# Optimization experiments

Measured on AMD Instinct MI355X. Metric: run time of the kernel, lower is better.

Reference implementation:

```python
import jax, jax.numpy as jnp
import numpy as np

HIDDEN = 1152
NUM_HEADS = 16
HEAD_DIM = HIDDEN // NUM_HEADS  # 72
BATCH, SEQ = 8, 1024


def setup_inputs() -> dict:
    key = jax.random.key(0)
    ks = jax.random.split(key, 9)
    s = 0.02
    return {
        "x": jax.random.normal(ks[0], (BATCH, SEQ, HIDDEN), dtype=jnp.float32),
        "wq": jax.random.normal(ks[1], (HIDDEN, HIDDEN), dtype=jnp.float32) * s,
        "bq": jax.random.normal(ks[2], (HIDDEN,), dtype=jnp.float32) * s,
        "wk": jax.random.normal(ks[3], (HIDDEN, HIDDEN), dtype=jnp.float32) * s,
        "bk": jax.random.normal(ks[4], (HIDDEN,), dtype=jnp.float32) * s,
        "wv": jax.random.normal(ks[5], (HIDDEN, HIDDEN), dtype=jnp.float32) * s,
        "bv": jax.random.normal(ks[6], (HIDDEN,), dtype=jnp.float32) * s,
        "wo": jax.random.normal(ks[7], (HIDDEN, HIDDEN), dtype=jnp.float32) * s,
        "bo": jax.random.normal(ks[8], (HIDDEN,), dtype=jnp.float32) * s,
    }


def reference(x, wq, bq, wk, bk, wv, bv, wo, bo):
    B, S, H = x.shape
    nh, hd = NUM_HEADS, HEAD_DIM
    # projections (weights stored [in, out] to match nn.Linear x @ W^T with W^T precomposed)
    q = (x @ wq + bq).reshape(B, S, nh, hd).transpose(0, 2, 1, 3)  # [B,nh,S,hd]
    k = (x @ wk + bk).reshape(B, S, nh, hd).transpose(0, 2, 1, 3)
    v = (x @ wv + bv).reshape(B, S, nh, hd).transpose(0, 2, 1, 3)
    scale = 1.0 / jnp.sqrt(jnp.asarray(hd, dtype=x.dtype))
    scores = jnp.einsum("bhqd,bhkd->bhqk", q, k) * scale  # [B,nh,S,S]
    attn = jax.nn.softmax(scores, axis=-1)
    out = jnp.einsum("bhqk,bhkd->bhqd", attn, v)  # [B,nh,S,hd]
    out = out.transpose(0, 2, 1, 3).reshape(B, S, H)
    return out @ wo + bo
```

## Files before the change

### kernel.cpp

```cpp
#include <hip/hip_runtime.h>
#include <hip/hip_bf16.h>

#define HIDDEN 1152
#define NUM_HEADS 16
#define BATCH 8
#define SEQ 1024
#define MROWS (BATCH * SEQ)
#define KSTRIDE 104
#define QSCALE_L2E (0.11785113019775793f * 1.4426950408889634f)

typedef __attribute__((ext_vector_type(8))) short short8;
typedef __attribute__((ext_vector_type(4))) float f32x4;

__device__ inline short f2bf(float x) {
  unsigned u = __float_as_uint(x);
  unsigned r = (u + 0x7FFFu + ((u >> 16) & 1u)) >> 16;
  return (short)(r & 0xFFFFu);
}

__device__ inline float fexp2(float x) { return __builtin_exp2f(x); }

__device__ inline void gload16(const void* g, void* l) {
  __builtin_amdgcn_global_load_lds(
      (const __attribute__((address_space(1))) void*)g,
      (__attribute__((address_space(3))) void*)l, 16, 0, 0);
}

__global__ __launch_bounds__(256) void k_prep(const float* __restrict__ X,
                                              short* __restrict__ Xb,
                                              short* __restrict__ Kp,
                                              short* __restrict__ Vt) {
  const int bid = blockIdx.x;
  if (bid < 4608) {
    const size_t base = ((size_t)bid * 256 + threadIdx.x) * 8;
    float4 a = *(const float4*)(X + base);
    float4 b = *(const float4*)(X + base + 4);
    short8 o = {f2bf(a.x), f2bf(a.y), f2bf(a.z), f2bf(a.w),
                f2bf(b.x), f2bf(b.y), f2bf(b.z), f2bf(b.w)};
    *(short8*)(Xb + base) = o;
  } else if (bid < 5120) {
    const int r = (bid - 4608) * 256 + threadIdx.x;
    const short8 z = {0, 0, 0, 0, 0, 0, 0, 0};
    short* p = Kp + (size_t)r * KSTRIDE + 72;
    *(short8*)(p) = z;
    *(short8*)(p + 8) = z;
    *(short8*)(p + 16) = z;
  } else {
    const int t = (bid - 5120) * 256 + threadIdx.x;
    const int bh = t >> 10;
    const int off = (t & 1023) * 8;
    const short o = ((t & 1023) >> 7) == 0 ? (short)0x3F80 : (short)0;
    short8 v = {o, o, o, o, o, o, o, o};
    *(short8*)(Vt + (size_t)bh * 81920 + 73728 + off) = v;
  }
}

__global__ __launch_bounds__(256) void k_cvtw(const float* __restrict__ W0,
                                              const float* __restrict__ W1,
                                              const float* __restrict__ W2,
                                              const float* __restrict__ W3,
                                              short* __restrict__ Wt) {
  __shared__ float T[64][65];
  const float* W = (blockIdx.z == 0) ? W0 : (blockIdx.z == 1) ? W1
                 : (blockIdx.z == 2) ? W2 : W3;
  short* dst = Wt + (size_t)blockIdx.z * HIDDEN * HIDDEN;
  const int n0 = blockIdx.x * 64, k0 = blockIdx.y * 64;
  const int tid = threadIdx.x;
  for (int t = tid; t < 4096; t += 256) {
    int r = t >> 6, c = t & 63;
    T[r][c] = W[(size_t)(k0 + r) * HIDDEN + n0 + c];
  }
  __syncthreads();
  for (int t = tid; t < 4096; t += 256) {
    int r = t >> 6, c = t & 63;
    dst[(size_t)(n0 + r) * HIDDEN + k0 + c] = f2bf(T[c][r]);
  }
}

__global__ __launch_bounds__(512) void k_gemm_qkv(
    const short* __restrict__ A, const short* __restrict__ Bt,
    const float* __restrict__ bq, const float* __restrict__ bk,
    const float* __restrict__ bv, short* __restrict__ Qb,
    short* __restrict__ Kp, short* __restrict__ Vt) {
  __shared__ __align__(16) short SM[24576];
  short* As = SM;
  short* Bs = SM + 16384;
  const int tid = threadIdx.x;
  const int lane = tid & 63;
  const int wid = tid >> 6;
  const int wr = wid >> 1, wc = wid & 1;
  const int flat = blockIdx.y * 27 + blockIdx.x;
  const int rid = (flat & 7) * 108 + (flat >> 3);
  const int row0 = (rid / 27) << 8;
  const int colTile = rid % 27;
  const int col0 = colTile << 7;
  const int l15 = lane & 15, lh = lane >> 4;
  const int lr8 = lane >> 3;
  const int csrc = ((lane & 7) ^ lr8) << 3;

  const f32x4 fz = {0.f, 0.f, 0.f, 0.f};
  f32x4 acc[4][4];
#pragma unroll
  for (int m = 0; m < 4; ++m)
#pragma unroll
    for (int n = 0; n < 4; ++n) acc[m][n] = fz;

  for (int k0 = 0; k0 < HIDDEN; k0 += 64) {
#pragma unroll
    for (int i = 0; i < 4; ++i) {
      const int c = (wid << 2) + i;
      const int r = (c << 3) + lr8;
      gload16(A + (size_t)(row0 + r) * HIDDEN + k0 + csrc, (void*)(As + (c << 9)));
    }
#pragma unroll
    for (int i = 0; i < 2; ++i) {
      const int c = (wid << 1) + i;
      const int r = (c << 3) + lr8;
      gload16(Bt + (size_t)(col0 + r) * HIDDEN + k0 + csrc, (void*)(Bs + (c << 9)));
    }
    __syncthreads();
#pragma unroll
    for (int ks = 0; ks < 2; ++ks) {
      short8 af[4], bfr[4];
#pragma unroll
      for (int m = 0; m < 4; ++m) {
        const int r = (wr << 6) + (m << 4) + l15;
        const int off = ((ks << 6) + (lh << 4)) ^ ((r & 7) << 4);
        af[m] = *(const short8*)((const char*)As + r * 128 + off);
      }
#pragma unroll
      for (int n = 0; n < 4; ++n) {
        const int r = (wc << 6) + (n << 4) + l15;
        const int off = ((ks << 6) + (lh << 4)) ^ ((r & 7) << 4);
        bfr[n] = *(const short8*)((const char*)Bs + r * 128 + off);
      }
      __builtin_amdgcn_s_setprio(1);
#pragma unroll
      for (int m = 0; m < 4; ++m)
#pragma unroll
        for (int n = 0; n < 4; ++n)
          acc[m][n] = __builtin_amdgcn_mfma_f32_16x16x32_bf16(af[m], bfr[n], acc[m][n], 0, 0, 0);
      __builtin_amdgcn_s_setprio(0);
    }
    __syncthreads();
  }

  const int cseg = colTile / 9;
  const int cwithin = (colTile % 9) << 7;
  if (cseg < 2) {
    short* dst = (cseg == 0) ? Qb : Kp;
    const float* bias = (cseg == 0) ? bq : bk;
    const float scl = (cseg == 0) ? QSCALE_L2E : 1.0f;
    const int rstride = (cseg == 0) ? 72 : KSTRIDE;
#pragma unroll
    for (int n = 0; n < 4; ++n) {
      const int c = cwithin + (wc << 6) + (n << 4) + l15;
      const int h = c / 72;
      const int d = c - h * 72;
      const float bvx = bias[c];
#pragma unroll
      for (int m = 0; m < 4; ++m)
#pragma unroll
        for (int i = 0; i < 4; ++i) {
          const int r = row0 + (wr << 6) + (m << 4) + (lh << 2) + i;
          const int b = r >> 10, s = r & 1023;
          dst[(size_t)((((b << 4) + h) << 10) + s) * rstride + d] =
              f2bf((acc[m][n][i] + bvx) * scl);
        }
    }
  } else {
    const int b = row0 >> 10;
    const int sb = row0 & 1023;
    short* Td = SM;
#pragma unroll
    for (int p = 0; p < 2; ++p) {
      if (wc == p) {
#pragma unroll
        for (int n = 0; n < 4; ++n) {
          const int ci = n * 16 + l15;
          const float bvx = bv[cwithin + p * 64 + ci];
#pragma unroll
          for (int m = 0; m < 4; ++m) {
            const int r0 = (wr << 6) + (m << 4) + (lh << 2);
            short4 o;
            o.x = f2bf(acc[m][n][0] + bvx);
            o.y = f2bf(acc[m][n][1] + bvx);
            o.z = f2bf(acc[m][n][2] + bvx);
            o.w = f2bf(acc[m][n][3] + bvx);
            *(short4*)(Td + ci * 264 + r0) = o;
          }
        }
      }
      __syncthreads();
      {
        const int ci = tid >> 3;
        const int part = tid & 7;
        const int cg = cwithin + p * 64 + ci;
        const int h = cg / 72;
        const int d = cg - h * 72;
        short* dstp = Vt + (((size_t)(((b << 4) + h) * 80 + d)) << 10) + sb + part * 32;
        const short* srcp = Td + ci * 264 + part * 32;
#pragma unroll
        for (int k = 0; k < 4; ++k)
          *(short8*)(dstp + k * 8) = *(const short8*)(srcp + k * 8);
      }
      __syncthreads();
    }
  }
}

__global__ __launch_bounds__(256) void k_gemm_o(const short* __restrict__ A,
                                                const short* __restrict__ Bt,
                                                const float* __restrict__ bias,
                                                float* __restrict__ C) {
  __shared__ __align__(16) short As[8192];
  __shared__ __align__(16) short Bs[8192];
  const int tid = threadIdx.x;
  const int lane = tid & 63;
  const int wid = tid >> 6;
  const int wr = wid >> 1, wc = wid & 1;
  const int flat = blockIdx.y * 9 + blockIdx.x;
  const int rid = (flat & 7) * 72 + (flat >> 3);
  const int row0 = (rid / 9) << 7;
  const int col0 = (rid % 9) << 7;
  const int l15 = lane & 15, lh = lane >> 4;
  const int lr8 = lane >> 3;
  const int csrc = ((lane & 7) ^ lr8) << 3;

  const f32x4 fz = {0.f, 0.f, 0.f, 0.f};
  f32x4 acc[4][4];
#pragma unroll
  for (int m = 0; m < 4; ++m)
#pragma unroll
    for (int n = 0; n < 4; ++n) acc[m][n] = fz;

  for (int k0 = 0; k0 < HIDDEN; k0 += 64) {
#pragma unroll
    for (int i = 0; i < 4; ++i) {
      const int chunk = (wid << 2) + i;
      const int r = (chunk << 3) + lr8;
      gload16(A + (size_t)(row0 + r) * HIDDEN + k0 + csrc, (void*)(As + (chunk << 9)));
      gload16(Bt + (size_t)(col0 + r) * HIDDEN + k0 + csrc, (void*)(Bs + (chunk << 9)));
    }
    __syncthreads();
#pragma unroll
    for (int ks = 0; ks < 2; ++ks) {
      short8 af[4], bfr[4];
#pragma unroll
      for (int m = 0; m < 4; ++m) {
        const int r = (wr << 6) + (m << 4) + l15;
        const int off = ((ks << 6) + (lh << 4)) ^ ((r & 7) << 4);
        af[m] = *(const short8*)((const char*)As + r * 128 + off);
      }
#pragma unroll
      for (int n = 0; n < 4; ++n) {
        const int r = (wc << 6) + (n << 4) + l15;
        const int off = ((ks << 6) + (lh << 4)) ^ ((r & 7) << 4);
        bfr[n] = *(const short8*)((const char*)Bs + r * 128 + off);
      }
      __builtin_amdgcn_s_setprio(1);
#pragma unroll
      for (int m = 0; m < 4; ++m)
#pragma unroll
        for (int n = 0; n < 4; ++n)
          acc[m][n] = __builtin_amdgcn_mfma_f32_16x16x32_bf16(af[m], bfr[n], acc[m][n], 0, 0, 0);
      __builtin_amdgcn_s_setprio(0);
    }
    __syncthreads();
  }

#pragma unroll
  for (int n = 0; n < 4; ++n) {
    const int c = col0 + (wc << 6) + (n << 4) + l15;
    const float bvx = bias[c];
#pragma unroll
    for (int m = 0; m < 4; ++m)
#pragma unroll
      for (int i = 0; i < 4; ++i) {
        const int r = row0 + (wr << 6) + (m << 4) + (lh << 2) + i;
        C[(size_t)r * HIDDEN + c] = acc[m][n][i] + bvx;
      }
  }
}

__global__ __launch_bounds__(256, 4) void k_attn(const short* __restrict__ Qg,
                                                 const short* __restrict__ Kp,
                                                 const short* __restrict__ Vt,
                                                 short* __restrict__ Og) {
  __shared__ __align__(16) short Ks[64 * KSTRIDE];
  __shared__ __align__(16) short Vs[80 * 64];
  __shared__ __align__(16) short Ps[4 * 16 * 72];
  const int tid = threadIdx.x, lane = tid & 63, wid = tid >> 6;
  const int l15 = lane & 15, lh = lane >> 4;
  const int id = blockIdx.x;
  const int rid = (id & 7) * 128 + (id >> 3);
  const int bh = rid >> 3;
  const int q0 = (rid & 7) << 7;
  const short8 sz = {0, 0, 0, 0, 0, 0, 0, 0};
  const f32x4 fz = {0.f, 0.f, 0.f, 0.f};

  short8 qf[2][3];
#pragma unroll
  for (int m = 0; m < 2; ++m)
#pragma unroll
    for (int ks = 0; ks < 3; ++ks) {
      const int row = q0 + wid * 32 + m * 16 + l15;
      const int e0 = ks * 32 + lh * 8;
      if (e0 < 72)
        qf[m][ks] = *(const short8*)(Qg + ((size_t)bh * 1024 + row) * 72 + e0);
      else
        qf[m][ks] = sz;
    }

  float mrun[2] = {-1e30f, -1e30f};
  f32x4 oacc[2][5];
#pragma unroll
  for (int m = 0; m < 2; ++m)
#pragma unroll
    for (int no = 0; no < 5; ++no) oacc[m][no] = fz;

  const char* kgb = (const char*)Kp + ((size_t)bh * 1024) * (KSTRIDE * 2);
  const char* vgb = (const char*)Vt + (size_t)bh * 163840;

  for (int kt = 0; kt < 16; ++kt) {
    const char* kg = kgb + (size_t)kt * 64 * (KSTRIDE * 2);
    for (int c = wid; c < 13; c += 4)
      gload16(kg + c * 1024 + lane * 16, (char*)Ks + c * 1024);
    for (int c = wid; c < 10; c += 4) {
      const int p = c * 1024 + lane * 16;
      const int d = p >> 7;
      const int sc16 = (lane & 7) ^ (d & 7);
      gload16(vgb + (size_t)d * 2048 + kt * 128 + sc16 * 16, (char*)Vs + c * 1024);
    }
    __syncthreads();

#pragma unroll
    for (int m = 0; m < 2; ++m) {
      f32x4 sa[4];
#pragma unroll
      for (int n = 0; n < 4; ++n) sa[n] = fz;
#pragma unroll
      for (int ks = 0; ks < 3; ++ks) {
        short8 kf[4];
#pragma unroll
        for (int n = 0; n < 4; ++n)
          kf[n] = *(const short8*)((const char*)Ks + (n * 16 + l15) * 208 + ks * 64 + lh * 16);
        __builtin_amdgcn_s_setprio(1);
#pragma unroll
        for (int n = 0; n < 4; ++n)
          sa[n] = __builtin_amdgcn_mfma_f32_16x16x32_bf16(kf[n], qf[m][ks], sa[n], 0, 0, 0);
        __builtin_amdgcn_s_setprio(0);
      }

#define M3(a, b, c) fmaxf(fmaxf((a), (b)), (c))
      float t0 = M3(sa[0][0], sa[0][1], sa[0][2]);
      float t1 = M3(sa[0][3], sa[1][0], sa[1][1]);
      float t2 = M3(sa[1][2], sa[1][3], sa[2][0]);
      float t3 = M3(sa[2][1], sa[2][2], sa[2][3]);
      float t4 = M3(sa[3][0], sa[3][1], sa[3][2]);
      float mx = fmaxf(M3(t0, t1, sa[3][3]), M3(t2, t3, t4));
#undef M3

      if (__any(mx > mrun[m] + 8.0f)) {
        mx = fmaxf(mx, __shfl_xor(mx, 16));
        mx = fmaxf(mx, __shfl_xor(mx, 32));
        const float nm = fmaxf(mrun[m], mx);
        const float corr = fexp2(mrun[m] - nm);
        mrun[m] = nm;
        float c0 = __shfl(corr, lh * 4 + 0);
        float c1 = __shfl(corr, lh * 4 + 1);
        float c2 = __shfl(corr, lh * 4 + 2);
        float c3 = __shfl(corr, lh * 4 + 3);
        const f32x4 cv = {c0, c1, c2, c3};
#pragma unroll
        for (int no = 0; no < 5; ++no) oacc[m][no] *= cv;
      }

#pragma unroll
      for (int n = 0; n < 4; ++n)
#pragma unroll
        for (int i = 0; i < 4; ++i) sa[n][i] = fexp2(sa[n][i] - mrun[m]);

#pragma unroll
      for (int n = 0; n < 4; ++n) {
        unsigned w0 = __builtin_amdgcn_perm(__float_as_uint(sa[n][1]),
                                            __float_as_uint(sa[n][0]), 0x07060302u);
        unsigned w1 = __builtin_amdgcn_perm(__float_as_uint(sa[n][3]),
                                            __float_as_uint(sa[n][2]), 0x07060302u);
        uint2 w = {w0, w1};
        *(uint2*)((char*)Ps + wid * 2304 + l15 * 144 + n * 32 + lh * 8) = w;
      }

#pragma unroll
      for (int ks = 0; ks < 2; ++ks) {
        const short8 pa = *(const short8*)((const char*)Ps + wid * 2304 + l15 * 144 + ks * 64 + lh * 16);
        short8 vb[5];
        const int cc = ((ks << 2) + lh) ^ (l15 & 7);
#pragma unroll
        for (int no = 0; no < 5; ++no)
          vb[no] = *(const short8*)((const char*)Vs + no * 2048 + l15 * 128 + cc * 16);
        __builtin_amdgcn_s_setprio(1);
#pragma unroll
        for (int no = 0; no < 5; ++no)
          oacc[m][no] = __builtin_amdgcn_mfma_f32_16x16x32_bf16(pa, vb[no], oacc[m][no], 0, 0, 0);
        __builtin_amdgcn_s_setprio(0);
      }
    }
    __syncthreads();
  }

  const int b = bh >> 4, h = bh & 15;
#pragma unroll
  for (int m = 0; m < 2; ++m) {
    float inv[4];
#pragma unroll
    for (int i = 0; i < 4; ++i)
      inv[i] = 1.0f / __shfl(oacc[m][4][i], (lane & 48) + 8);
#pragma unroll
    for (int no = 0; no < 5; ++no) {
      const int d = no * 16 + l15;
      if (d < 72) {
#pragma unroll
        for (int i = 0; i < 4; ++i) {
          const int s = q0 + wid * 32 + m * 16 + lh * 4 + i;
          Og[((size_t)(b * 1024 + s)) * HIDDEN + h * 72 + d] = f2bf(oacc[m][no][i] * inv[i]);
        }
      }
    }
  }
}

extern "C" void kernel_launch(void* const* d_in, const int* in_sizes, int n_in,
                              void* d_out, int out_size, void* d_ws, size_t ws_size,
                              hipStream_t stream) {
  const float* x  = (const float*)d_in[0];
  const float* wq = (const float*)d_in[1];
  const float* bq = (const float*)d_in[2];
  const float* wk = (const float*)d_in[3];
  const float* bk = (const float*)d_in[4];
  const float* wv = (const float*)d_in[5];
  const float* bv = (const float*)d_in[6];
  const float* wo = (const float*)d_in[7];
  const float* bo = (const float*)d_in[8];

  char* ws = (char*)d_ws;
  short* xb = (short*)ws;
  short* wT = (short*)(ws + 18874368);
  short* Qb = (short*)(ws + 29491200);
  short* Kp = (short*)(ws + 48365568);
  short* Vt = (short*)(ws + 75628544);
  const size_t WSZ = (size_t)HIDDEN * HIDDEN;

  k_prep<<<5632, 256, 0, stream>>>(x, xb, Kp, Vt);
  k_cvtw<<<dim3(18, 18, 4), 256, 0, stream>>>(wq, wk, wv, wo, wT);

  k_gemm_qkv<<<dim3(27, 32), 512, 0, stream>>>(xb, wT, bq, bk, bv, Qb, Kp, Vt);
  k_attn<<<1024, 256, 0, stream>>>(Qb, Kp, Vt, xb);
  k_gemm_o<<<dim3(9, 64), 256, 0, stream>>>(xb, wT + 3 * WSZ, bo, (float*)d_out);
}
```

Before: 217.2 us.

## Enlarge output GEMM tile to 256x128 and hoist QK^T MFMAs for both row blocks

The output projection GEMM now uses 512-thread blocks, each computing a 256x128 tile, so every B tile loaded from global memory is reused across twice as many rows and half as many blocks launch. Separately, the attention kernel computes QK^T scores for both 16-row sub-blocks before any softmax work, which reuses each K fragment loaded from LDS across two MFMAs and gives the scheduler more independent MFMAs. The hoisting keeps twice as many score registers live, which may reduce occupancy. The larger GEMM tile could also leave the grid too small to fill all CUs.

```diff
diff --git a/kernel.cpp b/kernel.cpp
--- a/kernel.cpp
+++ b/kernel.cpp
@@ -209,19 +209,20 @@
   }
 }
 
-__global__ __launch_bounds__(256) void k_gemm_o(const short* __restrict__ A,
+__global__ __launch_bounds__(512) void k_gemm_o(const short* __restrict__ A,
                                                 const short* __restrict__ Bt,
                                                 const float* __restrict__ bias,
                                                 float* __restrict__ C) {
-  __shared__ __align__(16) short As[8192];
-  __shared__ __align__(16) short Bs[8192];
+  __shared__ __align__(16) short SM[24576];
+  short* As = SM;
+  short* Bs = SM + 16384;
   const int tid = threadIdx.x;
   const int lane = tid & 63;
   const int wid = tid >> 6;
   const int wr = wid >> 1, wc = wid & 1;
   const int flat = blockIdx.y * 9 + blockIdx.x;
-  const int rid = (flat & 7) * 72 + (flat >> 3);
-  const int row0 = (rid / 9) << 7;
+  const int rid = (flat & 7) * 36 + (flat >> 3);
+  const int row0 = (rid / 9) << 8;
   const int col0 = (rid % 9) << 7;
   const int l15 = lane & 15, lh = lane >> 4;
   const int lr8 = lane >> 3;
@@ -237,10 +238,15 @@
   for (int k0 = 0; k0 < HIDDEN; k0 += 64) {
 #pragma unroll
     for (int i = 0; i < 4; ++i) {
-      const int chunk = (wid << 2) + i;
-      const int r = (chunk << 3) + lr8;
-      gload16(A + (size_t)(row0 + r) * HIDDEN + k0 + csrc, (void*)(As + (chunk << 9)));
-      gload16(Bt + (size_t)(col0 + r) * HIDDEN + k0 + csrc, (void*)(Bs + (chunk << 9)));
+      const int c = (wid << 2) + i;
+      const int r = (c << 3) + lr8;
+      gload16(A + (size_t)(row0 + r) * HIDDEN + k0 + csrc, (void*)(As + (c << 9)));
+    }
+#pragma unroll
+    for (int i = 0; i < 2; ++i) {
+      const int c = (wid << 1) + i;
+      const int r = (c << 3) + lr8;
+      gload16(Bt + (size_t)(col0 + r) * HIDDEN + k0 + csrc, (void*)(Bs + (c << 9)));
     }
     __syncthreads();
 #pragma unroll
@@ -321,6 +327,7 @@
 
   const char* kgb = (const char*)Kp + ((size_t)bh * 1024) * (KSTRIDE * 2);
   const char* vgb = (const char*)Vt + (size_t)bh * 163840;
+  short* psw = Ps + wid * 1152;
 
   for (int kt = 0; kt < 16; ++kt) {
     const char* kg = kgb + (size_t)kt * 64 * (KSTRIDE * 2);
@@ -334,31 +341,36 @@
     }
     __syncthreads();
 
+    f32x4 sa[2][4];
+#pragma unroll
+    for (int m = 0; m < 2; ++m)
+#pragma unroll
+      for (int n = 0; n < 4; ++n) sa[m][n] = fz;
+#pragma unroll
+    for (int ks = 0; ks < 3; ++ks) {
+      short8 kf[4];
+#pragma unroll
+      for (int n = 0; n < 4; ++n)
+        kf[n] = *(const short8*)((const char*)Ks + (n * 16 + l15) * 208 + ks * 64 + lh * 16);
+      __builtin_amdgcn_s_setprio(1);
+#pragma unroll
+      for (int n = 0; n < 4; ++n)
+        sa[0][n] = __builtin_amdgcn_mfma_f32_16x16x32_bf16(kf[n], qf[0][ks], sa[0][n], 0, 0, 0);
+#pragma unroll
+      for (int n = 0; n < 4; ++n)
+        sa[1][n] = __builtin_amdgcn_mfma_f32_16x16x32_bf16(kf[n], qf[1][ks], sa[1][n], 0, 0, 0);
+      __builtin_amdgcn_s_setprio(0);
+    }
+
 #pragma unroll
     for (int m = 0; m < 2; ++m) {
-      f32x4 sa[4];
-#pragma unroll
-      for (int n = 0; n < 4; ++n) sa[n] = fz;
-#pragma unroll
-      for (int ks = 0; ks < 3; ++ks) {
-        short8 kf[4];
-#pragma unroll
-        for (int n = 0; n < 4; ++n)
-          kf[n] = *(const short8*)((const char*)Ks + (n * 16 + l15) * 208 + ks * 64 + lh * 16);
-        __builtin_amdgcn_s_setprio(1);
-#pragma unroll
-        for (int n = 0; n < 4; ++n)
-          sa[n] = __builtin_amdgcn_mfma_f32_16x16x32_bf16(kf[n], qf[m][ks], sa[n], 0, 0, 0);
-        __builtin_amdgcn_s_setprio(0);
-      }
-
 #define M3(a, b, c) fmaxf(fmaxf((a), (b)), (c))
-      float t0 = M3(sa[0][0], sa[0][1], sa[0][2]);
-      float t1 = M3(sa[0][3], sa[1][0], sa[1][1]);
-      float t2 = M3(sa[1][2], sa[1][3], sa[2][0]);
-      float t3 = M3(sa[2][1], sa[2][2], sa[2][3]);
-      float t4 = M3(sa[3][0], sa[3][1], sa[3][2]);
-      float mx = fmaxf(M3(t0, t1, sa[3][3]), M3(t2, t3, t4));
+      float t0 = M3(sa[m][0][0], sa[m][0][1], sa[m][0][2]);
+      float t1 = M3(sa[m][0][3], sa[m][1][0], sa[m][1][1]);
+      float t2 = M3(sa[m][1][2], sa[m][1][3], sa[m][2][0]);
+      float t3 = M3(sa[m][2][1], sa[m][2][2], sa[m][2][3]);
+      float t4 = M3(sa[m][3][0], sa[m][3][1], sa[m][3][2]);
+      float mx = fmaxf(M3(t0, t1, sa[m][3][3]), M3(t2, t3, t4));
 #undef M3
 
       if (__any(mx > mrun[m] + 8.0f)) {
@@ -379,21 +391,21 @@
 #pragma unroll
       for (int n = 0; n < 4; ++n)
 #pragma unroll
-        for (int i = 0; i < 4; ++i) sa[n][i] = fexp2(sa[n][i] - mrun[m]);
+        for (int i = 0; i < 4; ++i) sa[m][n][i] = fexp2(sa[m][n][i] - mrun[m]);
 
 #pragma unroll
       for (int n = 0; n < 4; ++n) {
-        unsigned w0 = __builtin_amdgcn_perm(__float_as_uint(sa[n][1]),
-                                            __float_as_uint(sa[n][0]), 0x07060302u);
-        unsigned w1 = __builtin_amdgcn_perm(__float_as_uint(sa[n][3]),
-                                            __float_as_uint(sa[n][2]), 0x07060302u);
+        unsigned w0 = __builtin_amdgcn_perm(__float_as_uint(sa[m][n][1]),
+                                            __float_as_uint(sa[m][n][0]), 0x07060302u);
+        unsigned w1 = __builtin_amdgcn_perm(__float_as_uint(sa[m][n][3]),
+                                            __float_as_uint(sa[m][n][2]), 0x07060302u);
         uint2 w = {w0, w1};
-        *(uint2*)((char*)Ps + wid * 2304 + l15 * 144 + n * 32 + lh * 8) = w;
+        *(uint2*)((char*)psw + l15 * 144 + n * 32 + lh * 8) = w;
       }
 
 #pragma unroll
       for (int ks = 0; ks < 2; ++ks) {
-        const short8 pa = *(const short8*)((const char*)Ps + wid * 2304 + l15 * 144 + ks * 64 + lh * 16);
+        const short8 pa = *(const short8*)((const char*)psw + l15 * 144 + ks * 64 + lh * 16);
         short8 vb[5];
         const int cc = ((ks << 2) + lh) ^ (l15 & 7);
 #pragma unroll
@@ -456,5 +468,5 @@
 
   k_gemm_qkv<<<dim3(27, 32), 512, 0, stream>>>(xb, wT, bq, bk, bv, Qb, Kp, Vt);
   k_attn<<<1024, 256, 0, stream>>>(Qb, Kp, Vt, xb);
-  k_gemm_o<<<dim3(9, 64), 256, 0, stream>>>(xb, wT + 3 * WSZ, bo, (float*)d_out);
-}
+  k_gemm_o<<<dim3(9, 32), 512, 0, stream>>>(xb, wT + 3 * WSZ, bo, (float*)d_out);
+}
```

Measured after the change: 209.2 us. 1.04x faster.
